# Kernel tuning notes

Hardware: AMD Instinct MI355X
Metric: run time of the kernel (lower is better)

Reference implementation:

```python
import jax, jax.numpy as jnp
import numpy as np

N, K, C_IN, C_OUT = 100000, 16, 64, 64


def setup_inputs() -> dict:
    key = jax.random.key(0)
    ks = jax.random.split(key, 9)
    coords = jax.random.normal(ks[0], (N, 3), dtype=jnp.float32)
    features = jax.random.normal(ks[1], (N, C_IN), dtype=jnp.float32)
    idx = jax.random.randint(ks[2], (N, K), 0, N, dtype=jnp.int64)
    # kernel_mlp: Linear(3+C_IN, C_OUT) -> GELU -> Linear(C_OUT, C_OUT)
    s1 = 1.0 / np.sqrt(3 + C_IN)
    s2 = 1.0 / np.sqrt(C_OUT)
    W1 = jax.random.uniform(ks[3], (3 + C_IN, C_OUT), jnp.float32, -s1, s1)
    b1 = jax.random.uniform(ks[4], (C_OUT,), jnp.float32, -s1, s1)
    W2 = jax.random.uniform(ks[5], (C_OUT, C_OUT), jnp.float32, -s2, s2)
    b2 = jax.random.uniform(ks[6], (C_OUT,), jnp.float32, -s2, s2)
    sc = 1.0 / np.sqrt(C_IN)
    Ws = jax.random.uniform(ks[7], (C_IN, C_OUT), jnp.float32, -sc, sc)
    bs = jax.random.uniform(ks[8], (C_OUT,), jnp.float32, -sc, sc)
    return {"coords": coords, "features": features, "idx": idx,
            "W1": W1, "b1": b1, "W2": W2, "b2": b2, "Ws": Ws, "bs": bs}


def reference(coords, features, idx, W1, b1, W2, b2, Ws, bs):
    # gather neighbors: [N, K, 3] and [N, K, C_IN]
    neighbor_coords = coords[idx]
    neighbor_features = features[idx]
    rel_pos = neighbor_coords - coords[:, None, :]
    kernel_input = jnp.concatenate([rel_pos, neighbor_features], axis=-1)  # [N, K, 3+C_IN]
    h = jax.nn.gelu(kernel_input @ W1 + b1, approximate=False)  # torch GELU is exact erf
    kernel_out = h @ W2 + b2  # [N, K, C_OUT]
    aggregated = kernel_out.mean(axis=1)  # [N, C_OUT]
    return aggregated + features @ Ws + bs
```

## Files before the change

### kernel.cpp

```cpp
#include <hip/hip_runtime.h>
#include <hip/hip_fp16.h>
#include <math.h>


#define KNN 16

typedef _Float16 half8 __attribute__((ext_vector_type(8)));
typedef float float4v __attribute__((ext_vector_type(4)));
typedef int int4v __attribute__((ext_vector_type(4)));

__device__ __forceinline__ float lane_bcast(float v, int lane) {
    return __int_as_float(__builtin_amdgcn_readlane(__float_as_int(v), lane));
}

__device__ __forceinline__ float gelu_fast(float x) {
    const float t = x * fmaf(x * x, -0.10294324f, -2.30220821f);
    return x * __builtin_amdgcn_rcpf(1.0f + exp2f(t));
}

__global__ __launch_bounds__(256) void gno_phase1(
    const float* __restrict__ features, const float* __restrict__ coords,
    const float* __restrict__ W1, const float* __restrict__ b1,
    const float* __restrict__ Ws, const float* __restrict__ bs,
    const float* __restrict__ b2, __half* __restrict__ Gp,
    float* __restrict__ out, int n)
{
    const int c = threadIdx.x;
    float w1r[64], wsr[64];
    #pragma unroll
    for (int d = 0; d < 64; ++d) {
        w1r[d] = W1[(3 + d) * 64 + c];
        wsr[d] = Ws[d * 64 + c];
    }
    const float w1px = W1[c], w1py = W1[64 + c], w1pz = W1[128 + c];
    const float b1c = b1[c];
    const float sbc = bs[c] + b2[c];

    const int wave   = blockIdx.x * 4 + threadIdx.y;
    const int stride = gridDim.x * 4;
    for (int i0 = wave * 2; i0 < n; i0 += stride * 2) {
        const int i1 = i0 + 1;
        const bool has1 = (i1 < n);
        const float f0 = features[(size_t)i0 * 64 + c];
        const float f1 = has1 ? features[(size_t)i1 * 64 + c] : 0.0f;

        float a0 = fmaf(coords[(size_t)i0 * 3 + 0], w1px, b1c);
        a0 = fmaf(coords[(size_t)i0 * 3 + 1], w1py, a0);
        a0 = fmaf(coords[(size_t)i0 * 3 + 2], w1pz, a0);
        float a1 = b1c;
        if (has1) {
            a1 = fmaf(coords[(size_t)i1 * 3 + 0], w1px, a1);
            a1 = fmaf(coords[(size_t)i1 * 3 + 1], w1py, a1);
            a1 = fmaf(coords[(size_t)i1 * 3 + 2], w1pz, a1);
        }
        float s0 = sbc, s1 = sbc;
        #pragma unroll
        for (int d = 0; d < 64; ++d) {
            const float fd0 = lane_bcast(f0, d);
            const float fd1 = lane_bcast(f1, d);
            a0 = fmaf(fd0, w1r[d], a0);
            s0 = fmaf(fd0, wsr[d], s0);
            a1 = fmaf(fd1, w1r[d], a1);
            s1 = fmaf(fd1, wsr[d], s1);
        }
        Gp[(size_t)i0 * 64 + c]  = __float2half(a0);
        out[(size_t)i0 * 64 + c] = s0;
        if (has1) {
            Gp[(size_t)i1 * 64 + c]  = __float2half(a1);
            out[(size_t)i1 * 64 + c] = s1;
        }
    }
}

__global__ __launch_bounds__(256, 3) void gno_phase2(
    const float* __restrict__ coords, const int* __restrict__ idx,
    const float* __restrict__ W1, const float* __restrict__ W2,
    const __half2* __restrict__ Gp2, float* __restrict__ out, int n)
{
    __shared__ unsigned short w2h[4096];
    __shared__ unsigned short hbarall[4][1024];

    const int tid = threadIdx.y * 64 + threadIdx.x;
    for (int t = tid; t < 4096; t += 256)
        w2h[t] = __half_as_ushort(__float2half(W2[t]));

    const int c   = threadIdx.x;
    const int m   = c & 31;
    const int odd = c >> 5;
    const int p16 = c & 15;
    const int l4  = c >> 4;
    const int m4  = m * 4;
    const float wx0 = W1[2 * m],       wx1 = W1[2 * m + 1];
    const float wy0 = W1[64 + 2 * m],  wy1 = W1[64 + 2 * m + 1];
    const float wz0 = W1[128 + 2 * m], wz1 = W1[128 + 2 * m + 1];
    __syncthreads();

    half8 bf[4][2];
    #pragma unroll
    for (int t = 0; t < 4; ++t)
        #pragma unroll
        for (int h = 0; h < 2; ++h)
            #pragma unroll
            for (int j = 0; j < 8; ++j)
                bf[t][h][j] = *(const _Float16*)&w2h[(h * 32 + l4 * 8 + j) * 64 + t * 16 + p16];

    unsigned short* hb = hbarall[threadIdx.y];
    const char* gpb = (const char*)Gp2;

    const int ngroups = n >> 4;
    const int gw = blockIdx.x * 4 + threadIdx.y;
    const int nw = gridDim.x * 4;
    for (int g = gw; g < ngroups; g += nw) {
        const int gbase = g << 4;
        const int4v vj4 = *(const int4v*)(idx + (size_t)gbase * 16 + c * 4);
        const float cv = (c < 48) ? coords[(size_t)gbase * 3 + c] : 0.0f;

        #pragma unroll
        for (int h = 0; h < 2; ++h) {
            __half2 gv[4][16];
            #pragma unroll
            for (int pp = 0; pp < 4; ++pp) {
                const int P2 = h * 4 + pp;
                const int e0 = P2 * 32;
                #pragma unroll
                for (int q = 0; q < 8; ++q) {
                    const int ea = e0 + 2 * q,      eb = ea + 1;
                    const int ec = e0 + 16 + 2 * q, ed = ec + 1;
                    const int se = __builtin_amdgcn_readlane(vj4[ea & 3], ea >> 2);
                    const int so = __builtin_amdgcn_readlane(vj4[eb & 3], eb >> 2);
                    const int te = __builtin_amdgcn_readlane(vj4[ec & 3], ec >> 2);
                    const int td = __builtin_amdgcn_readlane(vj4[ed & 3], ed >> 2);
                    const int rA = odd ? so : se;
                    const int rB = odd ? td : te;
                    gv[pp][q]     = *(const __half2*)(gpb + (((unsigned)rA << 7) + m4));
                    gv[pp][8 + q] = *(const __half2*)(gpb + (((unsigned)rB << 7) + m4));
                }
            }
            #pragma unroll
            for (int pp = 0; pp < 4; ++pp) {
                const int P2  = h * 4 + pp;
                const int lp0 = 2 * P2;
                const float a0x = lane_bcast(cv, 3 * lp0 + 0);
                const float a0y = lane_bcast(cv, 3 * lp0 + 1);
                const float a0z = lane_bcast(cv, 3 * lp0 + 2);
                const float a1x = lane_bcast(cv, 3 * lp0 + 3);
                const float a1y = lane_bcast(cv, 3 * lp0 + 4);
                const float a1z = lane_bcast(cv, 3 * lp0 + 5);
                float P00 = a0x * wx0; P00 = fmaf(a0y, wy0, P00); P00 = fmaf(a0z, wz0, P00);
                float P01 = a0x * wx1; P01 = fmaf(a0y, wy1, P01); P01 = fmaf(a0z, wz1, P01);
                float P10 = a1x * wx0; P10 = fmaf(a1y, wy0, P10); P10 = fmaf(a1z, wz0, P10);
                float P11 = a1x * wx1; P11 = fmaf(a1y, wy1, P11); P11 = fmaf(a1z, wz1, P11);

                float a00 = 0.f, a01 = 0.f, a10 = 0.f, a11 = 0.f;
                #pragma unroll
                for (int q = 0; q < 8; ++q) {
                    const float2 xy = __half22float2(gv[pp][q]);
                    a00 += gelu_fast(xy.x - P00);
                    a01 += gelu_fast(xy.y - P01);
                }
                #pragma unroll
                for (int q = 0; q < 8; ++q) {
                    const float2 xy = __half22float2(gv[pp][8 + q]);
                    a10 += gelu_fast(xy.x - P10);
                    a11 += gelu_fast(xy.y - P11);
                }
                a00 *= (1.0f / KNN); a01 *= (1.0f / KNN);
                a10 *= (1.0f / KNN); a11 *= (1.0f / KNN);
                a00 += __shfl_xor(a00, 32, 64);
                a01 += __shfl_xor(a01, 32, 64);
                a10 += __shfl_xor(a10, 32, 64);
                a11 += __shfl_xor(a11, 32, 64);

                const int lp = lp0 + odd;
                const float x0 = odd ? a10 : a00;
                const float x1 = odd ? a11 : a01;
                __half2 hh = __floats2half2_rn(x0, x1);
                int byte = lp * 128 + m4;
                byte ^= (lp & 7) << 4;
                *(unsigned int*)((char*)hb + byte) = *(unsigned int*)&hh;
            }
        }

        int b0 = p16 * 128 + l4 * 16;       b0 ^= (p16 & 7) << 4;
        int b1 = p16 * 128 + 64 + l4 * 16;  b1 ^= (p16 & 7) << 4;
        const half8 af0 = *(const half8*)((const char*)hb + b0);
        const half8 af1 = *(const half8*)((const char*)hb + b1);

        #pragma unroll
        for (int t = 0; t < 4; ++t) {
            float4v cf;
            #pragma unroll
            for (int j = 0; j < 4; ++j)
                cf[j] = out[(size_t)(gbase + l4 * 4 + j) * 64 + t * 16 + p16];
            float4v d = __builtin_amdgcn_mfma_f32_16x16x32_f16(af0, bf[t][0], cf, 0, 0, 0);
            d = __builtin_amdgcn_mfma_f32_16x16x32_f16(af1, bf[t][1], d, 0, 0, 0);
            #pragma unroll
            for (int j = 0; j < 4; ++j)
                out[(size_t)(gbase + l4 * 4 + j) * 64 + t * 16 + p16] = d[j];
        }
    }
}

extern "C" void kernel_launch(void* const* d_in, const int* in_sizes, int n_in,
                              void* d_out, int out_size, void* d_ws, size_t ws_size,
                              hipStream_t stream) {
    const float* coords   = (const float*)d_in[0];
    const float* features = (const float*)d_in[1];
    const int*   idx      = (const int*)d_in[2];
    const float* W1       = (const float*)d_in[3];
    const float* b1       = (const float*)d_in[4];
    const float* W2       = (const float*)d_in[5];
    const float* b2       = (const float*)d_in[6];
    const float* Ws       = (const float*)d_in[7];
    const float* bs       = (const float*)d_in[8];
    float* out = (float*)d_out;
    const int n = in_sizes[0] / 3;
    __half* Gp = (__half*)d_ws;

    dim3 block(64, 4);
    gno_phase1<<<dim3(1024), block, 0, stream>>>(features, coords, W1, b1,
                                                 Ws, bs, b2, Gp, out, n);
    gno_phase2<<<dim3(782),  block, 0, stream>>>(coords, idx, W1, W2,
                                                 (const __half2*)Gp, out, n);
}
```

Baseline: 201.7 us.

## Move phase-1 feature projections onto fp16 MFMA with permuted Gp channel layout

Phase 1 now takes tiles of 16 points, stages their features in swizzled LDS as fp16, and computes both the W1 projection and the Ws skip projection with 16x16x32 MFMA instead of per-lane readlane FMAs. Gp is written with a permuted channel order, and phase 2 remaps its W1 coordinate weights and W2 B-fragment rows to match. Launch sizes change (phase1 782 blocks, phase2 1563) and phase 1 gets an occupancy hint. The skip path is now computed from fp16-rounded features and weights, which adds precision loss.

```diff
diff --git a/kernel.cpp b/kernel.cpp
--- a/kernel.cpp
+++ b/kernel.cpp
@@ -18,56 +18,108 @@
     return x * __builtin_amdgcn_rcpf(1.0f + exp2f(t));
 }
 
-__global__ __launch_bounds__(256) void gno_phase1(
+__device__ __forceinline__ int sigma_ch(int kp) {
+    const int mm = kp >> 1;
+    const int base = (mm & 1) ? ((mm >> 1) + 32) : (mm >> 1);
+    return base + ((kp & 1) ? 16 : 0);
+}
+
+__device__ __forceinline__ unsigned int pack_h2(float a, float b) {
+    const __half2 h = __floats2half2_rn(a, b);
+    return __builtin_bit_cast(unsigned int, h);
+}
+
+__global__ __launch_bounds__(256, 4) void gno_phase1(
     const float* __restrict__ features, const float* __restrict__ coords,
     const float* __restrict__ W1, const float* __restrict__ b1,
     const float* __restrict__ Ws, const float* __restrict__ bs,
     const float* __restrict__ b2, __half* __restrict__ Gp,
     float* __restrict__ out, int n)
 {
-    const int c = threadIdx.x;
-    float w1r[64], wsr[64];
+    __shared__ unsigned short fstage[4][1024];
+    const int c   = threadIdx.x;
+    const int p16 = c & 15;
+    const int l4  = c >> 4;
+
+    half8 bfG[4][2], bfS[4][2];
     #pragma unroll
-    for (int d = 0; d < 64; ++d) {
-        w1r[d] = W1[(3 + d) * 64 + c];
-        wsr[d] = Ws[d * 64 + c];
-    }
-    const float w1px = W1[c], w1py = W1[64 + c], w1pz = W1[128 + c];
-    const float b1c = b1[c];
-    const float sbc = bs[c] + b2[c];
-
-    const int wave   = blockIdx.x * 4 + threadIdx.y;
-    const int stride = gridDim.x * 4;
-    for (int i0 = wave * 2; i0 < n; i0 += stride * 2) {
-        const int i1 = i0 + 1;
-        const bool has1 = (i1 < n);
-        const float f0 = features[(size_t)i0 * 64 + c];
-        const float f1 = has1 ? features[(size_t)i1 * 64 + c] : 0.0f;
-
-        float a0 = fmaf(coords[(size_t)i0 * 3 + 0], w1px, b1c);
-        a0 = fmaf(coords[(size_t)i0 * 3 + 1], w1py, a0);
-        a0 = fmaf(coords[(size_t)i0 * 3 + 2], w1pz, a0);
-        float a1 = b1c;
-        if (has1) {
-            a1 = fmaf(coords[(size_t)i1 * 3 + 0], w1px, a1);
-            a1 = fmaf(coords[(size_t)i1 * 3 + 1], w1py, a1);
-            a1 = fmaf(coords[(size_t)i1 * 3 + 2], w1pz, a1);
-        }
-        float s0 = sbc, s1 = sbc;
-        #pragma unroll
-        for (int d = 0; d < 64; ++d) {
-            const float fd0 = lane_bcast(f0, d);
-            const float fd1 = lane_bcast(f1, d);
-            a0 = fmaf(fd0, w1r[d], a0);
-            s0 = fmaf(fd0, wsr[d], s0);
-            a1 = fmaf(fd1, w1r[d], a1);
-            s1 = fmaf(fd1, wsr[d], s1);
-        }
-        Gp[(size_t)i0 * 64 + c]  = __float2half(a0);
-        out[(size_t)i0 * 64 + c] = s0;
-        if (has1) {
-            Gp[(size_t)i1 * 64 + c]  = __float2half(a1);
-            out[(size_t)i1 * 64 + c] = s1;
+    for (int t = 0; t < 4; ++t) {
+        const int col = t * 16 + p16;
+        #pragma unroll
+        for (int h = 0; h < 2; ++h)
+            #pragma unroll
+            for (int j = 0; j < 8; ++j) {
+                const int kp = h * 32 + l4 * 8 + j;
+                bfG[t][h][j] = (_Float16)W1[(3 + kp) * 64 + col];
+                bfS[t][h][j] = (_Float16)Ws[kp * 64 + col];
+            }
+    }
+    float w1x[4], w1y[4], w1z[4], b1v[4], sbv[4];
+    #pragma unroll
+    for (int t = 0; t < 4; ++t) {
+        const int col = t * 16 + p16;
+        w1x[t] = W1[col]; w1y[t] = W1[64 + col]; w1z[t] = W1[128 + col];
+        b1v[t] = b1[col]; sbv[t] = bs[col] + b2[col];
+    }
+    unsigned short* fs = fstage[threadIdx.y];
+
+    const int ngroups = n >> 4;
+    const int gw = blockIdx.x * 4 + threadIdx.y;
+    const int nw = gridDim.x * 4;
+    for (int g = gw; g < ngroups; g += nw) {
+        const int gbase = g << 4;
+        float f[16];
+        #pragma unroll
+        for (int p = 0; p < 16; ++p) f[p] = features[(size_t)(gbase + p) * 64 + c];
+        #pragma unroll
+        for (int p = 0; p < 16; ++p) {
+            const int byte = (p * 128) + ((c * 2) ^ ((p & 7) << 4));
+            *(unsigned short*)((char*)fs + byte) =
+                __half_as_ushort(__float2half(f[p]));
+        }
+        const float cv = (c < 48) ? coords[(size_t)gbase * 3 + c] : 0.0f;
+
+        const int bo0 = (p16 * 128 + l4 * 16) ^ ((p16 & 7) << 4);
+        const int bo1 = (p16 * 128 + 64 + l4 * 16) ^ ((p16 & 7) << 4);
+        const half8 af0 = *(const half8*)((const char*)fs + bo0);
+        const half8 af1 = *(const half8*)((const char*)fs + bo1);
+
+        float4v cfG[4];
+        #pragma unroll
+        for (int j = 0; j < 4; ++j) {
+            const int lp = l4 * 4 + j;
+            const float cx = __shfl(cv, 3 * lp + 0, 64);
+            const float cy = __shfl(cv, 3 * lp + 1, 64);
+            const float cz = __shfl(cv, 3 * lp + 2, 64);
+            #pragma unroll
+            for (int t = 0; t < 4; ++t) {
+                float v = fmaf(cx, w1x[t], b1v[t]);
+                v = fmaf(cy, w1y[t], v);
+                v = fmaf(cz, w1z[t], v);
+                cfG[t][j] = v;
+            }
+        }
+
+        float4v dG[4];
+        #pragma unroll
+        for (int t = 0; t < 4; ++t) {
+            float4v cs = {sbv[t], sbv[t], sbv[t], sbv[t]};
+            float4v dS = __builtin_amdgcn_mfma_f32_16x16x32_f16(af0, bfS[t][0], cs, 0, 0, 0);
+            dS = __builtin_amdgcn_mfma_f32_16x16x32_f16(af1, bfS[t][1], dS, 0, 0, 0);
+            float4v dg = __builtin_amdgcn_mfma_f32_16x16x32_f16(af0, bfG[t][0], cfG[t], 0, 0, 0);
+            dg = __builtin_amdgcn_mfma_f32_16x16x32_f16(af1, bfG[t][1], dg, 0, 0, 0);
+            dG[t] = dg;
+            #pragma unroll
+            for (int j = 0; j < 4; ++j)
+                out[(size_t)(gbase + l4 * 4 + j) * 64 + t * 16 + p16] = dS[j];
+        }
+        #pragma unroll
+        for (int j = 0; j < 4; ++j) {
+            const unsigned long long v =
+                (unsigned long long)pack_h2(dG[0][j], dG[1][j]) |
+                ((unsigned long long)pack_h2(dG[2][j], dG[3][j]) << 32);
+            *(unsigned long long*)((char*)Gp +
+                (size_t)(gbase + l4 * 4 + j) * 128 + p16 * 8) = v;
         }
     }
 }
@@ -90,9 +142,11 @@
     const int p16 = c & 15;
     const int l4  = c >> 4;
     const int m4  = m * 4;
-    const float wx0 = W1[2 * m],       wx1 = W1[2 * m + 1];
-    const float wy0 = W1[64 + 2 * m],  wy1 = W1[64 + 2 * m + 1];
-    const float wz0 = W1[128 + 2 * m], wz1 = W1[128 + 2 * m + 1];
+    const int cA = (m & 1) ? ((m >> 1) + 32) : (m >> 1);
+    const int cB = cA + 16;
+    const float wx0 = W1[cA],       wx1 = W1[cB];
+    const float wy0 = W1[64 + cA],  wy1 = W1[64 + cB];
+    const float wz0 = W1[128 + cA], wz1 = W1[128 + cB];
     __syncthreads();
 
     half8 bf[4][2];
@@ -102,7 +156,8 @@
         for (int h = 0; h < 2; ++h)
             #pragma unroll
             for (int j = 0; j < 8; ++j)
-                bf[t][h][j] = *(const _Float16*)&w2h[(h * 32 + l4 * 8 + j) * 64 + t * 16 + p16];
+                bf[t][h][j] = *(const _Float16*)
+                    &w2h[sigma_ch(h * 32 + l4 * 8 + j) * 64 + t * 16 + p16];
 
     unsigned short* hb = hbarall[threadIdx.y];
     const char* gpb = (const char*)Gp2;
@@ -174,15 +229,15 @@
                 const int lp = lp0 + odd;
                 const float x0 = odd ? a10 : a00;
                 const float x1 = odd ? a11 : a01;
-                __half2 hh = __floats2half2_rn(x0, x1);
+                const unsigned int hh = pack_h2(x0, x1);
                 int byte = lp * 128 + m4;
                 byte ^= (lp & 7) << 4;
-                *(unsigned int*)((char*)hb + byte) = *(unsigned int*)&hh;
-            }
-        }
-
-        int b0 = p16 * 128 + l4 * 16;       b0 ^= (p16 & 7) << 4;
-        int b1 = p16 * 128 + 64 + l4 * 16;  b1 ^= (p16 & 7) << 4;
+                *(unsigned int*)((char*)hb + byte) = hh;
+            }
+        }
+
+        const int b0 = (p16 * 128 + l4 * 16) ^ ((p16 & 7) << 4);
+        const int b1 = (p16 * 128 + 64 + l4 * 16) ^ ((p16 & 7) << 4);
         const half8 af0 = *(const half8*)((const char*)hb + b0);
         const half8 af1 = *(const half8*)((const char*)hb + b1);
 
@@ -218,8 +273,8 @@
     __half* Gp = (__half*)d_ws;
 
     dim3 block(64, 4);
-    gno_phase1<<<dim3(1024), block, 0, stream>>>(features, coords, W1, b1,
+    gno_phase1<<<dim3(782),  block, 0, stream>>>(features, coords, W1, b1,
                                                  Ws, bs, b2, Gp, out, n);
-    gno_phase2<<<dim3(782),  block, 0, stream>>>(coords, idx, W1, W2,
+    gno_phase2<<<dim3(1563), block, 0, stream>>>(coords, idx, W1, W2,
                                                  (const __half2*)Gp, out, n);
 }
```

New measurement: 216.7 us. +7.4%, slower.
